# Performance work log

Hardware: AMD Instinct MI355X
Metric: run time of the kernel (lower is better)

The kernel has to match this reference:

```python
import jax, jax.numpy as jnp
import numpy as np

NUM_GRAPHS = 1024


def setup_inputs() -> dict:
    key = jax.random.key(0)
    k1, k2, k3, k4 = jax.random.split(key, 4)
    N, D, H = 500000, 256, 128
    x = jax.random.normal(k1, (N, D), dtype=jnp.float32)
    # attention MLP params (Linear(D,H) -> ReLU -> Linear(H,1))
    W1 = jax.random.normal(k2, (D, H), dtype=jnp.float32) * (1.0 / np.sqrt(D))
    b1 = jnp.zeros((H,), dtype=jnp.float32)
    W2 = jax.random.normal(k3, (H, 1), dtype=jnp.float32) * (1.0 / np.sqrt(H))
    b2 = jnp.zeros((1,), dtype=jnp.float32)
    batch = jnp.sort(jax.random.randint(k4, (N,), 0, NUM_GRAPHS)).astype(jnp.int64)
    return {"x": x, "W1": W1, "b1": b1, "W2": W2, "b2": b2, "batch": batch}


def reference(x, W1, b1, W2, b2, batch):
    # attention MLP -> scalar score per node, softmax over ALL nodes (global, as in source)
    h = jax.nn.relu(x @ W1 + b1)            # [N, H]
    scores = h @ W2 + b2                    # [N, 1]
    attn = jax.nn.softmax(scores.ravel())[:, None]  # [N, 1], global softmax

    # attention-weighted sum per graph
    attn_pooled = jax.ops.segment_sum(x * attn, batch, num_segments=NUM_GRAPHS,
                                      indices_are_sorted=True)  # [G, D]
    # max pool per graph (all segments occupied given N >> G)
    max_pooled = jax.ops.segment_max(x, batch, num_segments=NUM_GRAPHS,
                                     indices_are_sorted=True)   # [G, D]
    # mean pool per graph: scatter-add + clamped counts
    sum_pooled = jax.ops.segment_sum(x, batch, num_segments=NUM_GRAPHS,
                                     indices_are_sorted=True)   # [G, D]
    counts = jnp.bincount(batch, length=NUM_GRAPHS).astype(x.dtype)
    counts = jnp.clip(counts, 1.0, None)[:, None]                # [G, 1]
    mean_pooled = sum_pooled / counts

    return jnp.concatenate([attn_pooled, max_pooled, mean_pooled], axis=-1)  # [G, 3D]
```

## Files before the change

### kernel.cpp

```cpp
#include <hip/hip_runtime.h>
#include <cmath>

#define D_IN 256
#define H_DIM 128
#define NUM_GRAPHS 1024
#define CHUNK 64
#define MAXSEG 4
#define REC_F 768

typedef __attribute__((ext_vector_type(8))) __bf16 bf16x8;
typedef __attribute__((ext_vector_type(4))) float f32x4;
typedef __attribute__((ext_vector_type(4))) unsigned short ushort4v;

__device__ inline float b2f(unsigned short u) {
    unsigned int v = ((unsigned int)u) << 16;
    return __builtin_bit_cast(float, v);
}

__global__ void pack_w1(const float* __restrict__ W1, ushort* __restrict__ packed) {
    int tid = blockIdx.x * 256 + threadIdx.x;
    if (tid >= 8 * 8 * 64) return;
    int nt = tid >> 9;
    int ks = (tid >> 6) & 7;
    int l = tid & 63;
    int col = nt * 16 + (l & 15);
    int kbase = ks * 32 + ((l >> 4) & 3) * 8;
#pragma unroll
    for (int i = 0; i < 8; ++i) {
        float v = W1[(size_t)(kbase + i) * H_DIM + col];
        __bf16 b = (__bf16)v;
        packed[(size_t)tid * 8 + i] = __builtin_bit_cast(unsigned short, b);
    }
}

__global__ __launch_bounds__(256) void fused_kernel(
    const float* __restrict__ x, const ushort* __restrict__ w1p,
    const float* __restrict__ b1, const float* __restrict__ W2,
    const float* __restrict__ b2, const int* __restrict__ batch,
    float* __restrict__ recs, int2* __restrict__ hdr,
    float* __restrict__ zpart, int N) {
    int tid = threadIdx.x;
    int l = tid & 63;
    int w = tid >> 6;
    int r16 = l & 15;
    int kg = l >> 4;
    int blk = blockIdx.x;
    long long base = (long long)blk * CHUNK;
    int chunkN = (int)min((long long)CHUNK, (long long)N - base);

    __shared__ ushort sx[CHUNK * D_IN];
    __shared__ float pscore[CHUNK][4];
    __shared__ int sbatch[CHUNK];
    __shared__ int seglist[MAXSEG + 1];
    __shared__ int seggid[MAXSEG];
    __shared__ int snseg;

    int bval = 0;
    if (w == 0) {
        long long bi = base + l;
        bval = (bi < N) ? batch[bi] : -1;
        sbatch[l] = bval;
    }

    bf16x8 breg0[8], breg1[8];
#pragma unroll
    for (int ks = 0; ks < 8; ++ks) {
        breg0[ks] = *(const bf16x8*)(w1p + ((size_t)((w * 2) * 8 + ks) * 64 + l) * 8);
        breg1[ks] = *(const bf16x8*)(w1p + ((size_t)((w * 2 + 1) * 8 + ks) * 64 + l) * 8);
    }

    {
        int row = tid >> 2;
        long long grow = base + row;
        if (grow >= N) grow = N - 1;
        const float* xr = x + grow * D_IN;
        int gb = tid & 3;
        f32x4 xv[16];
#pragma unroll
        for (int j = 0; j < 8; ++j) {
            int g = gb + 4 * j;
            xv[2 * j] = *(const f32x4*)(xr + g * 8);
            xv[2 * j + 1] = *(const f32x4*)(xr + g * 8 + 4);
        }
        unsigned rowswz = (unsigned)(row & 7) << 4;
#pragma unroll
        for (int j = 0; j < 8; ++j) {
            int g = gb + 4 * j;
            bf16x8 pk;
#pragma unroll
            for (int i = 0; i < 4; ++i) {
                pk[i] = (__bf16)xv[2 * j][i];
                pk[i + 4] = (__bf16)xv[2 * j + 1][i];
            }
            unsigned addr = ((unsigned)(row * 512 + g * 16)) ^ rowswz;
            *(bf16x8*)((char*)sx + addr) = pk;
        }
    }

    float w2v[2], b1v[2];
#pragma unroll
    for (int q = 0; q < 2; ++q) {
        int c = (w * 2 + q) * 16 + r16;
        w2v[q] = W2[c];
        b1v[q] = b1[c];
    }
    float bb = b2[0];

    if (w == 0) {
        int prev = __shfl_up(bval, 1, 64);
        bool flag = (l < chunkN) && (l == 0 || bval != prev);
        unsigned long long m = __ballot(flag);
        if (l == 0) {
            int ns = 0;
            while (m && ns < MAXSEG) {
                int b = __ffsll(m) - 1;
                seglist[ns] = b;
                seggid[ns] = sbatch[b];
                ns++;
                m &= m - 1;
            }
            snseg = ns;
            seglist[ns] = chunkN;
        }
    }
    __syncthreads();

    f32x4 acc[4][2] = {};
#pragma unroll
    for (int ks = 0; ks < 8; ++ks) {
#pragma unroll
        for (int mt = 0; mt < 4; ++mt) {
            int row = mt * 16 + r16;
            unsigned addr = ((unsigned)(row * 512 + ks * 64 + kg * 16)) ^
                            ((unsigned)(row & 7) << 4);
            bf16x8 af = *(const bf16x8*)((const char*)sx + addr);
            acc[mt][0] = __builtin_amdgcn_mfma_f32_16x16x32_bf16(af, breg0[ks], acc[mt][0], 0, 0, 0);
            acc[mt][1] = __builtin_amdgcn_mfma_f32_16x16x32_bf16(af, breg1[ks], acc[mt][1], 0, 0, 0);
        }
    }
#pragma unroll
    for (int mt = 0; mt < 4; ++mt) {
#pragma unroll
        for (int reg = 0; reg < 4; ++reg) {
            float p = fmaxf(acc[mt][0][reg] + b1v[0], 0.f) * w2v[0] +
                      fmaxf(acc[mt][1][reg] + b1v[1], 0.f) * w2v[1];
            p += __shfl_xor(p, 1, 64);
            p += __shfl_xor(p, 2, 64);
            p += __shfl_xor(p, 4, 64);
            p += __shfl_xor(p, 8, 64);
            if (r16 == 0) pscore[mt * 16 + kg * 4 + reg][w] = p;
        }
    }
    __syncthreads();

    f32x4 ps = *(const f32x4*)&pscore[l][0];
    float e_l = (l < chunkN) ? __expf(ps[0] + ps[1] + ps[2] + ps[3] + bb) : 0.f;

    if (w == 0) {
        float z = e_l;
        z += __shfl_xor(z, 1, 64);
        z += __shfl_xor(z, 2, 64);
        z += __shfl_xor(z, 4, 64);
        z += __shfl_xor(z, 8, 64);
        z += __shfl_xor(z, 16, 64);
        z += __shfl_xor(z, 32, 64);
        if (l == 0) zpart[blk] = z;
    }

    int nseg = snseg;

    f32x4 asum = {0.f, 0.f, 0.f, 0.f};
    f32x4 ssum = {0.f, 0.f, 0.f, 0.f};
    f32x4 mx = {-INFINITY, -INFINITY, -INFINITY, -INFINITY};

    for (int sg = 0; sg < nseg; ++sg) {
        int sStart = seglist[sg];
        int sEnd = seglist[sg + 1];
#pragma unroll
        for (int j = 0; j < 16; ++j) {
            int row = w * 16 + j;
            float wj = __shfl(e_l, row, 64);
            bool in = (row >= sStart) && (row < sEnd);
            unsigned addr = ((unsigned)(row * 512 + l * 8)) ^
                            ((unsigned)(row & 7) << 4);
            ushort4v hv = *(const ushort4v*)((const char*)sx + addr);
            float wje = in ? wj : 0.f;
#pragma unroll
            for (int c = 0; c < 4; ++c) {
                float v = b2f(hv[c]);
                asum[c] += v * wje;
                ssum[c] += in ? v : 0.f;
                mx[c] = fmaxf(mx[c], in ? v : -INFINITY);
            }
        }
        float* rb = recs + ((size_t)(blk * MAXSEG + sg) * 4 + w) * REC_F;
        *(f32x4*)(rb + l * 4) = asum;
        *(f32x4*)(rb + 256 + l * 4) = ssum;
        *(f32x4*)(rb + 512 + l * 4) = mx;
        if (w == 0 && l == 0)
            hdr[blk * MAXSEG + sg] = make_int2(seggid[sg], sEnd - sStart);
#pragma unroll
        for (int c = 0; c < 4; ++c) {
            asum[c] = 0.f;
            ssum[c] = 0.f;
            mx[c] = -INFINITY;
        }
    }
    if (w == 0 && l == 0) {
        for (int sg = nseg; sg < MAXSEG; ++sg)
            hdr[blk * MAXSEG + sg] = make_int2(-1, 0);
    }
}

__global__ __launch_bounds__(256) void zreduce_kernel(
    const float* __restrict__ zpart, int n, float* __restrict__ MZ) {
    int tid = threadIdx.x;
    float z = 0.f;
    for (int i = tid; i < n; i += 256) z += zpart[i];
    __shared__ float sz[256];
    sz[tid] = z;
    __syncthreads();
    for (int off = 128; off > 0; off >>= 1) {
        if (tid < off) sz[tid] += sz[tid + off];
        __syncthreads();
    }
    if (tid == 0) MZ[0] = 1.f / sz[0];
}

__device__ inline int lower_bound_i(const int* __restrict__ arr, int n, int val) {
    int lo = 0, hi = n;
    while (lo < hi) {
        int mid = (lo + hi) >> 1;
        if (arr[mid] < val) lo = mid + 1; else hi = mid;
    }
    return lo;
}

__global__ __launch_bounds__(256) void combine_kernel(
    const float* __restrict__ recs, const int2* __restrict__ hdr,
    const float* __restrict__ MZ,
    const int* __restrict__ batch, int N, float* __restrict__ out) {
    int g = blockIdx.x;
    int tid = threadIdx.x;
    int w = tid >> 6;
    int l = tid & 63;
    float invZ = MZ[0];

    __shared__ int sb[2];
    if (tid < 2) sb[tid] = lower_bound_i(batch, N, g + tid);
    __syncthreads();
    int start = sb[0], end = sb[1];

    f32x4 ew = {0.f, 0.f, 0.f, 0.f};
    f32x4 ss = {0.f, 0.f, 0.f, 0.f};
    f32x4 mxv = {-INFINITY, -INFINITY, -INFINITY, -INFINITY};
    int cnt = 0;
    if (end > start) {
        int b0 = start >> 6, b1 = (end - 1) >> 6;
        for (int b = b0; b <= b1; ++b) {
#pragma unroll
            for (int sg = 0; sg < MAXSEG; ++sg) {
                int2 h = hdr[b * MAXSEG + sg];
                if (h.x == g) {
                    const float* rb = recs + ((size_t)(b * MAXSEG + sg) * 4 + w) * REC_F;
                    f32x4 a = *(const f32x4*)(rb + l * 4);
                    f32x4 s = *(const f32x4*)(rb + 256 + l * 4);
                    f32x4 m = *(const f32x4*)(rb + 512 + l * 4);
#pragma unroll
                    for (int c = 0; c < 4; ++c) {
                        ew[c] += a[c];
                        ss[c] += s[c];
                        mxv[c] = fmaxf(mxv[c], m[c]);
                    }
                    cnt += h.y;
                }
            }
        }
    }

    __shared__ float red[4][3][256];
    *(f32x4*)&red[w][0][l * 4] = ew;
    *(f32x4*)&red[w][1][l * 4] = ss;
    *(f32x4*)&red[w][2][l * 4] = mxv;
    __syncthreads();
    float ewt = red[0][0][tid] + red[1][0][tid] + red[2][0][tid] + red[3][0][tid];
    float sst = red[0][1][tid] + red[1][1][tid] + red[2][1][tid] + red[3][1][tid];
    float mxt = fmaxf(fmaxf(red[0][2][tid], red[1][2][tid]),
                      fmaxf(red[2][2][tid], red[3][2][tid]));

    size_t ob = (size_t)g * (3 * D_IN);
    out[ob + tid] = ewt * invZ;
    out[ob + D_IN + tid] = (end > start) ? mxt : 0.f;
    out[ob + 2 * D_IN + tid] = sst / (float)max(cnt, 1);
}

extern "C" void kernel_launch(void* const* d_in, const int* in_sizes, int n_in,
                              void* d_out, int out_size, void* d_ws, size_t ws_size,
                              hipStream_t stream) {
    const float* x = (const float*)d_in[0];
    const float* W1 = (const float*)d_in[1];
    const float* b1 = (const float*)d_in[2];
    const float* W2 = (const float*)d_in[3];
    const float* b2 = (const float*)d_in[4];
    const int* batch = (const int*)d_in[5];
    int N = in_sizes[0] / D_IN;
    float* out = (float*)d_out;
    int NB = (N + CHUNK - 1) / CHUNK;

    char* ws = (char*)d_ws;
    size_t off = 0;
    ushort* w1p = (ushort*)(ws + off);
    off += 8 * 8 * 64 * 8 * sizeof(ushort);
    off = (off + 255) & ~(size_t)255;
    float* recs = (float*)(ws + off);
    off += (size_t)NB * MAXSEG * 4 * REC_F * sizeof(float);
    off = (off + 255) & ~(size_t)255;
    int2* hdr = (int2*)(ws + off);
    off += (size_t)NB * MAXSEG * sizeof(int2);
    off = (off + 255) & ~(size_t)255;
    float* zpart = (float*)(ws + off);
    off += (size_t)NB * sizeof(float);
    off = (off + 255) & ~(size_t)255;
    float* MZ = (float*)(ws + off);
    off += 256;

    pack_w1<<<16, 256, 0, stream>>>(W1, w1p);
    fused_kernel<<<NB, 256, 0, stream>>>(x, w1p, b1, W2, b2, batch,
                                         recs, hdr, zpart, N);
    zreduce_kernel<<<1, 256, 0, stream>>>(zpart, NB, MZ);
    combine_kernel<<<NUM_GRAPHS, 256, 0, stream>>>(recs, hdr, MZ, batch, N, out);
}
```

Measured before the change: 172.8 us.

## Reduce per-wave partial records in LDS before writing to global memory

The fused kernel now combines the four per-wave segment partials (weighted sum, sum, max) through shared memory and writes a single 768-float record per segment instead of four. This cuts the global write traffic for the partial records and the matching reads in the combine kernel by a factor of four, and the combine kernel no longer needs its own cross-wave LDS reduction. In exchange, each segment iteration in the fused kernel gains two block-wide barriers and 12 KB of extra shared memory, which could lower occupancy.

```diff
diff --git a/kernel.cpp b/kernel.cpp
--- a/kernel.cpp
+++ b/kernel.cpp
@@ -50,6 +50,7 @@
 
     __shared__ ushort sx[CHUNK * D_IN];
     __shared__ float pscore[CHUNK][4];
+    __shared__ float red[4][3][256];
     __shared__ int sbatch[CHUNK];
     __shared__ int seglist[MAXSEG + 1];
     __shared__ int seggid[MAXSEG];
@@ -193,12 +194,25 @@
                 mx[c] = fmaxf(mx[c], in ? v : -INFINITY);
             }
         }
-        float* rb = recs + ((size_t)(blk * MAXSEG + sg) * 4 + w) * REC_F;
-        *(f32x4*)(rb + l * 4) = asum;
-        *(f32x4*)(rb + 256 + l * 4) = ssum;
-        *(f32x4*)(rb + 512 + l * 4) = mx;
-        if (w == 0 && l == 0)
+        *(f32x4*)&red[w][0][l * 4] = asum;
+        *(f32x4*)&red[w][1][l * 4] = ssum;
+        *(f32x4*)&red[w][2][l * 4] = mx;
+        __syncthreads();
+        {
+            float aa = red[0][0][tid] + red[1][0][tid] +
+                       red[2][0][tid] + red[3][0][tid];
+            float s2 = red[0][1][tid] + red[1][1][tid] +
+                       red[2][1][tid] + red[3][1][tid];
+            float m2 = fmaxf(fmaxf(red[0][2][tid], red[1][2][tid]),
+                             fmaxf(red[2][2][tid], red[3][2][tid]));
+            float* rb = recs + (size_t)(blk * MAXSEG + sg) * REC_F;
+            rb[tid] = aa;
+            rb[256 + tid] = s2;
+            rb[512 + tid] = m2;
+        }
+        if (tid == 0)
             hdr[blk * MAXSEG + sg] = make_int2(seggid[sg], sEnd - sStart);
+        __syncthreads();
 #pragma unroll
         for (int c = 0; c < 4; ++c) {
             asum[c] = 0.f;
@@ -206,7 +220,7 @@
             mx[c] = -INFINITY;
         }
     }
-    if (w == 0 && l == 0) {
+    if (tid == 0) {
         for (int sg = nseg; sg < MAXSEG; ++sg)
             hdr[blk * MAXSEG + sg] = make_int2(-1, 0);
     }
@@ -242,8 +256,6 @@
     const int* __restrict__ batch, int N, float* __restrict__ out) {
     int g = blockIdx.x;
     int tid = threadIdx.x;
-    int w = tid >> 6;
-    int l = tid & 63;
     float invZ = MZ[0];
 
     __shared__ int sb[2];
@@ -251,9 +263,7 @@
     __syncthreads();
     int start = sb[0], end = sb[1];
 
-    f32x4 ew = {0.f, 0.f, 0.f, 0.f};
-    f32x4 ss = {0.f, 0.f, 0.f, 0.f};
-    f32x4 mxv = {-INFINITY, -INFINITY, -INFINITY, -INFINITY};
+    float ew = 0.f, ss = 0.f, mxv = -INFINITY;
     int cnt = 0;
     if (end > start) {
         int b0 = start >> 6, b1 = (end - 1) >> 6;
@@ -262,36 +272,19 @@
             for (int sg = 0; sg < MAXSEG; ++sg) {
                 int2 h = hdr[b * MAXSEG + sg];
                 if (h.x == g) {
-                    const float* rb = recs + ((size_t)(b * MAXSEG + sg) * 4 + w) * REC_F;
-                    f32x4 a = *(const f32x4*)(rb + l * 4);
-                    f32x4 s = *(const f32x4*)(rb + 256 + l * 4);
-                    f32x4 m = *(const f32x4*)(rb + 512 + l * 4);
-#pragma unroll
-                    for (int c = 0; c < 4; ++c) {
-                        ew[c] += a[c];
-                        ss[c] += s[c];
-                        mxv[c] = fmaxf(mxv[c], m[c]);
-                    }
+                    const float* rb = recs + (size_t)(b * MAXSEG + sg) * REC_F;
+                    ew += rb[tid];
+                    ss += rb[256 + tid];
+                    mxv = fmaxf(mxv, rb[512 + tid]);
                     cnt += h.y;
                 }
             }
         }
     }
-
-    __shared__ float red[4][3][256];
-    *(f32x4*)&red[w][0][l * 4] = ew;
-    *(f32x4*)&red[w][1][l * 4] = ss;
-    *(f32x4*)&red[w][2][l * 4] = mxv;
-    __syncthreads();
-    float ewt = red[0][0][tid] + red[1][0][tid] + red[2][0][tid] + red[3][0][tid];
-    float sst = red[0][1][tid] + red[1][1][tid] + red[2][1][tid] + red[3][1][tid];
-    float mxt = fmaxf(fmaxf(red[0][2][tid], red[1][2][tid]),
-                      fmaxf(red[2][2][tid], red[3][2][tid]));
-
     size_t ob = (size_t)g * (3 * D_IN);
-    out[ob + tid] = ewt * invZ;
-    out[ob + D_IN + tid] = (end > start) ? mxt : 0.f;
-    out[ob + 2 * D_IN + tid] = sst / (float)max(cnt, 1);
+    out[ob + tid] = ew * invZ;
+    out[ob + D_IN + tid] = (end > start) ? mxv : 0.f;
+    out[ob + 2 * D_IN + tid] = ss / (float)max(cnt, 1);
 }
 
 extern "C" void kernel_launch(void* const* d_in, const int* in_sizes, int n_in,
@@ -313,7 +306,7 @@
     off += 8 * 8 * 64 * 8 * sizeof(ushort);
     off = (off + 255) & ~(size_t)255;
     float* recs = (float*)(ws + off);
-    off += (size_t)NB * MAXSEG * 4 * REC_F * sizeof(float);
+    off += (size_t)NB * MAXSEG * REC_F * sizeof(float);
     off = (off + 255) & ~(size_t)255;
     int2* hdr = (int2*)(ws + off);
     off += (size_t)NB * MAXSEG * sizeof(int2);
```

After: 181.3 us. +4.9%, slower.
